# Optimization experiments

Measured on AMD Instinct MI355X. Metric: run time of the kernel, lower is better.

## Reference

```python
import jax, jax.numpy as jnp
import numpy as np

EPS = 1e-5
NEG_SLOPE = 0.2

def _conv1x1(x, w):
    # x: (B,C,N,K), w: (O,C) -> (B,O,N,K)
    return jnp.einsum('oc,bcnk->bonk', w, x)

def _bn(x, g, b, m, v):
    scale = g / jnp.sqrt(v + EPS)
    return x * scale[None, :, None, None] + (b - m * scale)[None, :, None, None]

def _lrelu(x):
    return jnp.where(x > 0, x, NEG_SLOPE * x)

def setup_inputs() -> dict:
    key = jax.random.key(0)
    specs = {
        'x': ((8, 6, 8192, 20), 'randn'),
        'trans_w': ((64, 6), 'randn'), 'trans_g': ((64,), 'rand'), 'trans_b': ((64,), 'randn'),
        'trans_m': ((64,), 'randn'), 'trans_v': ((64,), 'rand'),
        'pos_w1': ((64, 3), 'randn'), 'pos_g': ((64,), 'rand'), 'pos_b': ((64,), 'randn'),
        'pos_m': ((64,), 'randn'), 'pos_v': ((64,), 'rand'),
        'pos_w2': ((64, 64), 'randn'), 'pos_b2': ((64,), 'randn'),
        'gate_w1': ((16, 6), 'randn'), 'gate_g': ((16,), 'rand'), 'gate_b': ((16,), 'randn'),
        'gate_m': ((16,), 'randn'), 'gate_v': ((16,), 'rand'),
        'gate_w2': ((1, 16), 'randn'), 'gate_b2': ((1,), 'ones'),
        'attn_w1': ((16, 6), 'randn'), 'attn_g': ((16,), 'rand'), 'attn_b': ((16,), 'randn'),
        'attn_m': ((16,), 'randn'), 'attn_v': ((16,), 'rand'),
        'attn_w2': ((64, 16), 'randn'), 'attn_b2': ((64,), 'randn'),
    }
    out = {}
    for i, (name, (shape, fill)) in enumerate(specs.items()):
        k = jax.random.fold_in(key, i)
        if fill == 'randn':
            out[name] = jax.random.normal(k, shape, dtype=jnp.float32) * 0.1
        elif fill == 'rand':
            out[name] = jax.random.uniform(k, shape, dtype=jnp.float32)
        else:  # ones (gate bias init to 2.0 in original; scale ones)
            out[name] = jnp.ones(shape, dtype=jnp.float32) * 2.0
    return out

def reference(x, trans_w, trans_g, trans_b, trans_m, trans_v,
              pos_w1, pos_g, pos_b, pos_m, pos_v, pos_w2, pos_b2,
              gate_w1, gate_g, gate_b, gate_m, gate_v, gate_w2, gate_b2,
              attn_w1, attn_g, attn_b, attn_m, attn_v, attn_w2, attn_b2):
    in_channels = 3
    rel_pos = x[:, in_channels:in_channels + 3, :, :]  # (B,3,N,K)
    # pos_net: conv(3->C) + BN + LReLU + conv(C->C, bias)
    pos_h = _lrelu(_bn(_conv1x1(rel_pos, pos_w1), pos_g, pos_b, pos_m, pos_v))
    pos_enc = _conv1x1(pos_h, pos_w2) + pos_b2[None, :, None, None]
    # trans: conv(2*Cin->C) + BN + LReLU
    trans_feat = _lrelu(_bn(_conv1x1(x, trans_w), trans_g, trans_b, trans_m, trans_v)) + pos_enc
    # gate_net: conv(6->16)+BN+LReLU+conv(16->1,bias)+sigmoid (dropout=0 in eval)
    gate_h = _lrelu(_bn(_conv1x1(x, gate_w1), gate_g, gate_b, gate_m, gate_v))
    gate_map = jax.nn.sigmoid(_conv1x1(gate_h, gate_w2) + gate_b2[None, :, None, None])  # (B,1,N,K)
    clean_feat = trans_feat * gate_map
    # attn_net: conv(6->16)+BN+LReLU+conv(16->C,bias), then + pos_enc, softmax over K
    attn_h = _lrelu(_bn(_conv1x1(x, attn_w1), attn_g, attn_b, attn_m, attn_v))
    attn_logits = _conv1x1(attn_h, attn_w2) + attn_b2[None, :, None, None] + pos_enc
    attn_weights = jax.nn.softmax(attn_logits, axis=-1)
    out_attn = (trans_feat * attn_weights).sum(axis=-1)  # (B,C,N)
    out_max = clean_feat.max(axis=-1)                    # (B,C,N)
    return out_attn + out_max
```

## Files before the change

kernel.cpp:

```cpp
#include <hip/hip_runtime.h>
#include <math.h>

#define NEG 0.2f
#define EPSV 1e-5f

typedef _Float16 v8h __attribute__((ext_vector_type(8)));
typedef _Float16 v4h __attribute__((ext_vector_type(4)));
typedef _Float16 v2h __attribute__((ext_vector_type(2)));
typedef __fp16   f16x2 __attribute__((ext_vector_type(2)));
typedef float    v4f __attribute__((ext_vector_type(4)));

__device__ __forceinline__ float lrelu(float v) { return fmaxf(v, NEG * v); }
__device__ __forceinline__ v4f lrelu4(v4f v) {
    return __builtin_elementwise_max(v, v * NEG);
}
__device__ __forceinline__ v2h lreluh2(v2h v) {
    return __builtin_elementwise_max(v, v * (_Float16)NEG);
}

__device__ __forceinline__ v2h pk(float a, float b) {
    union { f16x2 i; v2h o; } u;
    u.i = __builtin_amdgcn_cvt_pkrtz(a, b);
    return u.o;
}

#define MFMA16(a, b, c) __builtin_amdgcn_mfma_f32_16x16x16f16((a), (b), (c), 0, 0, 0)

__global__ __launch_bounds__(256, 4)
void gsl_mfma(const float* __restrict__ x,
              const float* __restrict__ trans_w, const float* __restrict__ trans_g,
              const float* __restrict__ trans_b, const float* __restrict__ trans_m,
              const float* __restrict__ trans_v,
              const float* __restrict__ pos_w1, const float* __restrict__ pos_g,
              const float* __restrict__ pos_b, const float* __restrict__ pos_m,
              const float* __restrict__ pos_v, const float* __restrict__ pos_w2,
              const float* __restrict__ pos_b2,
              const float* __restrict__ gate_w1, const float* __restrict__ gate_g,
              const float* __restrict__ gate_b, const float* __restrict__ gate_m,
              const float* __restrict__ gate_v, const float* __restrict__ gate_w2,
              const float* __restrict__ gate_b2,
              const float* __restrict__ attn_w1, const float* __restrict__ attn_g,
              const float* __restrict__ attn_b, const float* __restrict__ attn_m,
              const float* __restrict__ attn_v, const float* __restrict__ attn_w2,
              const float* __restrict__ attn_b2,
              float* __restrict__ out)
{
    __shared__ _Float16 WH[1920];
    __shared__ _Float16 W2L[5120];
    __shared__ float    PB2[64];

    const int tid  = threadIdx.x;
    const int wv   = tid >> 6;
    const int lane = tid & 63;
    const int p    = lane & 15;
    const int q    = lane >> 4;

    const int b  = blockIdx.x >> 7;
    const int n0 = ((blockIdx.x & 127) << 6) | (wv << 4);
    const int n  = n0 | p;

    #pragma unroll
    for (int e = 0; e < 16; ++e) {
        int idx = tid * 16 + e;
        int t   = idx >> 9;
        int rem = idx & 511;
        int pp  = rem >> 5;
        int ii  = rem & 31;
        int c   = (t & 1) * 32 + ((ii & 7) >> 2) * 16 + ((ii >> 3) << 2) + (ii & 3);
        W2L[t * 640 + pp * 40 + ii] =
            (_Float16)pos_w2[((t >> 1) * 16 + pp) * 64 + c];
    }

    if (tid < 64) {
        const int c = tid;
        float sp = pos_g[c] * rsqrtf(pos_v[c] + EPSV);
        float bp = pos_b[c] - pos_m[c] * sp;
        _Float16* row = WH + (c >> 4) * 320 + (c & 15) * 20;
        for (int k = 0; k < 20; ++k) {
            float v = (k >= 3 && k < 6) ? pos_w1[c * 3 + (k - 3)] * sp
                                        : ((k == 6) ? bp : 0.f);
            row[k] = (_Float16)v;
        }
        PB2[c] = pos_b2[c];
    } else if (tid < 80) {
        const int j = tid - 64;
        float sa = attn_g[j] * rsqrtf(attn_v[j] + EPSV);
        float ba = attn_b[j] - attn_m[j] * sa;
        _Float16* row = WH + 1280 + j * 20;
        for (int k = 0; k < 20; ++k)
            row[k] = (_Float16)((k < 6) ? attn_w1[j * 6 + k] * sa
                                        : ((k == 6) ? ba : 0.f));
    } else if (tid < 96) {
        const int j = tid - 80;
        float sg = gate_g[j] * rsqrtf(gate_v[j] + EPSV);
        float bg = gate_b[j] - gate_m[j] * sg;
        _Float16* row = WH + 1600 + j * 20;
        for (int k = 0; k < 20; ++k)
            row[k] = (_Float16)((k < 6) ? gate_w1[j * 6 + k] * sg
                                        : ((k == 6) ? bg : 0.f));
    }

    v4h WTf[4], WA2f[4], WG2f;
    #pragma unroll
    for (int mt = 0; mt < 4; ++mt) {
        const int ch = mt * 16 + p;
        #pragma unroll
        for (int i = 0; i < 4; ++i)
            WA2f[mt][i] = (_Float16)attn_w2[ch * 16 + q * 4 + i];
        float st = trans_g[ch] * rsqrtf(trans_v[ch] + EPSV);
        float bt = trans_b[ch] - trans_m[ch] * st;
        #pragma unroll
        for (int i = 0; i < 4; ++i) {
            int k = q * 4 + i;
            float v = (k < 6) ? trans_w[ch * 6 + k] * st : ((k == 6) ? bt : 0.f);
            WTf[mt][i] = (_Float16)v;
        }
    }
    #pragma unroll
    for (int i = 0; i < 4; ++i)
        WG2f[i] = (_Float16)gate_w2[4 * q + i];
    const float gb2v = gate_b2[0];

    __syncthreads();

    const _Float16* const WP1p = WH + p * 20 + q * 4;
    const _Float16* const WA1p = WH + 1280 + p * 20 + q * 4;
    const _Float16* const WG1p = WH + 1600 + p * 20 + q * 4;
    const _Float16* const W2Lp = W2L + p * 40 + q * 8;
    const float* const    PB2p = PB2 + 4 * q;

    const v4f zero = {0.f, 0.f, 0.f, 0.f};
    v4f den[4], num[4], cmx[4];
    #pragma unroll
    for (int mt = 0; mt < 4; ++mt) {
        den[mt] = zero; num[mt] = zero;
        cmx[mt] = (v4f){-3.4e38f, -3.4e38f, -3.4e38f, -3.4e38f};
    }

    const float* xb = x + ((size_t)(b * 6) * 8192 + n) * 20;
    const int hi = q & 1;
    const float* const s0p = xb + (size_t)(hi ? 4 : 0) * 163840;
    const float* const s1p = xb + (size_t)(hi ? 5 : 1) * 163840;
    const float* const s2p = xb + (size_t)(hi ? 4 : 2) * 163840;
    const float* const s3p = xb + (size_t)(hi ? 5 : 3) * 163840;

    auto mk = [&](float a, float bb, float cc, float dd) -> v4h {
        v2h lo = pk(a, bb);
        v2h hh = pk(cc, dd);
        if (hi) { union { unsigned u; v2h h; } t; t.u = 0x00003C00u; hh = t.h; }
        return (v4h){lo.x, lo.y, hh.x, hh.y};
    };

    float c0 = s0p[0], c1 = s1p[0], c2 = s2p[0], c3 = s3p[0];

    #pragma unroll 1
    for (int k = 0; k < 20; ++k) {
        asm volatile("" ::: "memory");

        v4h xv = mk(c0, c1, c2, c3);
        if (k < 19) {
            c0 = s0p[k + 1]; c1 = s1p[k + 1];
            c2 = s2p[k + 1]; c3 = s3p[k + 1];
        }

        v4h phB[4];
        #pragma unroll
        for (int mt = 0; mt < 4; ++mt) {
            v4f php = MFMA16(*(const v4h*)(WP1p + mt * 320), xv, zero);
            union { v4h v; v2h h[2]; } u;
            u.h[0] = lreluh2(pk(php[0], php[1]));
            u.h[1] = lreluh2(pk(php[2], php[3]));
            phB[mt] = u.v;
        }
        v4f ahp = MFMA16(*(const v4h*)WA1p, xv, zero);
        union { v4h v; v2h h[2]; } ua;
        ua.h[0] = lreluh2(pk(ahp[0], ahp[1]));
        ua.h[1] = lreluh2(pk(ahp[2], ahp[3]));
        const v4h ahB = ua.v;

        v4f ghp = MFMA16(*(const v4h*)WG1p, xv, zero);
        union { v4h v; v2h h[2]; } ug;
        ug.h[0] = lreluh2(pk(ghp[0], ghp[1]));
        ug.h[1] = lreluh2(pk(ghp[2], ghp[3]));
        v4f gav = MFMA16(WG2f, ug.v, zero);
        const float gate = 1.f / (1.f + __expf(-(gav[0] + gb2v)));

        #pragma unroll
        for (int mt = 0; mt < 4; ++mt) {
            union { v8h v; v4h h[2]; } w2a, w2b;
            w2a.v = *(const v8h*)(W2Lp + (mt * 2 + 0) * 640);
            w2b.v = *(const v8h*)(W2Lp + (mt * 2 + 1) * 640);
            v4f pe = MFMA16(w2a.h[0], phB[0], *(const v4f*)(PB2p + mt * 16));
            pe = MFMA16(w2a.h[1], phB[1], pe);
            pe = MFMA16(w2b.h[0], phB[2], pe);
            pe = MFMA16(w2b.h[1], phB[3], pe);
            v4f tfa = MFMA16(WTf[mt], xv, zero);
            v4f tfv = lrelu4(tfa) + pe;
            pe = MFMA16(WA2f[mt], ahB, pe);
            v4f e;
            #pragma unroll
            for (int r = 0; r < 4; ++r) e[r] = __expf(pe[r]);
            den[mt] += e;
            num[mt] += tfv * e;
            cmx[mt] = __builtin_elementwise_max(cmx[mt], tfv * gate);
        }
    }

    #pragma unroll
    for (int mt = 0; mt < 4; ++mt) {
        #pragma unroll
        for (int r = 0; r < 4; ++r) {
            const int ch = mt * 16 + 4 * q + r;
            out[((size_t)(b * 64 + ch)) * 8192 + n] =
                num[mt][r] / den[mt][r] + cmx[mt][r];
        }
    }
}

extern "C" void kernel_launch(void* const* d_in, const int* in_sizes, int n_in,
                              void* d_out, int out_size, void* d_ws, size_t ws_size,
                              hipStream_t stream) {
    const float* x       = (const float*)d_in[0];
    const float* trans_w = (const float*)d_in[1];
    const float* trans_g = (const float*)d_in[2];
    const float* trans_b = (const float*)d_in[3];
    const float* trans_m = (const float*)d_in[4];
    const float* trans_v = (const float*)d_in[5];
    const float* pos_w1  = (const float*)d_in[6];
    const float* pos_g   = (const float*)d_in[7];
    const float* pos_b   = (const float*)d_in[8];
    const float* pos_m   = (const float*)d_in[9];
    const float* pos_v   = (const float*)d_in[10];
    const float* pos_w2  = (const float*)d_in[11];
    const float* pos_b2  = (const float*)d_in[12];
    const float* gate_w1 = (const float*)d_in[13];
    const float* gate_g  = (const float*)d_in[14];
    const float* gate_b  = (const float*)d_in[15];
    const float* gate_m  = (const float*)d_in[16];
    const float* gate_v  = (const float*)d_in[17];
    const float* gate_w2 = (const float*)d_in[18];
    const float* gate_b2 = (const float*)d_in[19];
    const float* attn_w1 = (const float*)d_in[20];
    const float* attn_g  = (const float*)d_in[21];
    const float* attn_b  = (const float*)d_in[22];
    const float* attn_m  = (const float*)d_in[23];
    const float* attn_v  = (const float*)d_in[24];
    const float* attn_w2 = (const float*)d_in[25];
    const float* attn_b2 = (const float*)d_in[26];
    float* out = (float*)d_out;

    gsl_mfma<<<1024, 256, 0, stream>>>(
        x, trans_w, trans_g, trans_b, trans_m, trans_v,
        pos_w1, pos_g, pos_b, pos_m, pos_v, pos_w2, pos_b2,
        gate_w1, gate_g, gate_b, gate_m, gate_v, gate_w2, gate_b2,
        attn_w1, attn_g, attn_b, attn_m, attn_v, attn_w2, attn_b2,
        out);
}
```

Baseline: 176.1 us.

## Split the K reduction across wave pairs and merge partial softmax sums via LDS

Each block now covers 32 points instead of 64. Two waves share a 16-point group and each handles half of the 20 neighbours, so the grid doubles to 2048 blocks. At the end, partial denominators, numerators and maxima are combined through an LDS buffer that reuses the weight shared memory, using extra barriers. Launch bounds are raised to 8 blocks per CU. The aim is more parallelism and shorter serial k-loops per wave. The cost is redundant weight staging per block, extra synchronisation, and register pressure from the tighter launch bound.

Result: slower. 351.5 us (+99.6%).

```diff
diff --git a/kernel.cpp b/kernel.cpp
--- a/kernel.cpp
+++ b/kernel.cpp
@@ -26,7 +26,7 @@
 
 #define MFMA16(a, b, c) __builtin_amdgcn_mfma_f32_16x16x16f16((a), (b), (c), 0, 0, 0)
 
-__global__ __launch_bounds__(256, 4)
+__global__ __launch_bounds__(256, 8)
 void gsl_mfma(const float* __restrict__ x,
               const float* __restrict__ trans_w, const float* __restrict__ trans_g,
               const float* __restrict__ trans_b, const float* __restrict__ trans_m,
@@ -45,9 +45,10 @@
               const float* __restrict__ attn_b2,
               float* __restrict__ out)
 {
-    __shared__ _Float16 WH[1920];
-    __shared__ _Float16 W2L[5120];
-    __shared__ float    PB2[64];
+    __shared__ __align__(16) char SMEM[14336];
+    _Float16* const WH  = (_Float16*)SMEM;
+    _Float16* const W2L = (_Float16*)(SMEM + 3840);
+    float*    const PB2 = (float*)(SMEM + 14080);
 
     const int tid  = threadIdx.x;
     const int wv   = tid >> 6;
@@ -55,8 +56,11 @@
     const int p    = lane & 15;
     const int q    = lane >> 4;
 
-    const int b  = blockIdx.x >> 7;
-    const int n0 = ((blockIdx.x & 127) << 6) | (wv << 4);
+    const int pw = wv & 1;
+    const int kh = wv >> 1;
+
+    const int b  = blockIdx.x >> 8;
+    const int n0 = ((blockIdx.x & 255) << 5) | (pw << 4);
     const int n  = n0 | p;
 
     #pragma unroll
@@ -151,16 +155,17 @@
         return (v4h){lo.x, lo.y, hh.x, hh.y};
     };
 
-    float c0 = s0p[0], c1 = s1p[0], c2 = s2p[0], c3 = s3p[0];
+    const int k0 = kh * 10;
+    float c0 = s0p[k0], c1 = s1p[k0], c2 = s2p[k0], c3 = s3p[k0];
 
     #pragma unroll 1
-    for (int k = 0; k < 20; ++k) {
+    for (int j = 0; j < 10; ++j) {
         asm volatile("" ::: "memory");
 
         v4h xv = mk(c0, c1, c2, c3);
-        if (k < 19) {
-            c0 = s0p[k + 1]; c1 = s1p[k + 1];
-            c2 = s2p[k + 1]; c3 = s3p[k + 1];
+        if (j < 9) {
+            const int kn = k0 + j + 1;
+            c0 = s0p[kn]; c1 = s1p[kn]; c2 = s2p[kn]; c3 = s3p[kn];
         }
 
         v4h phB[4];
@@ -206,13 +211,60 @@
         }
     }
 
-    #pragma unroll
-    for (int mt = 0; mt < 4; ++mt) {
-        #pragma unroll
-        for (int r = 0; r < 4; ++r) {
-            const int ch = mt * 16 + 4 * q + r;
-            out[((size_t)(b * 64 + ch)) * 8192 + n] =
-                num[mt][r] / den[mt][r] + cmx[mt][r];
+    __syncthreads();
+    float* const XBUF = (float*)SMEM;
+
+    if (wv == 2) {
+        float* dst = XBUF + lane * 48;
+        #pragma unroll
+        for (int mt = 0; mt < 4; ++mt) {
+            *(v4f*)(dst + mt * 4)      = den[mt];
+            *(v4f*)(dst + 16 + mt * 4) = num[mt];
+            *(v4f*)(dst + 32 + mt * 4) = cmx[mt];
+        }
+    }
+    __syncthreads();
+    if (wv == 0) {
+        const float* src = XBUF + lane * 48;
+        #pragma unroll
+        for (int mt = 0; mt < 4; ++mt) {
+            den[mt] += *(const v4f*)(src + mt * 4);
+            num[mt] += *(const v4f*)(src + 16 + mt * 4);
+            cmx[mt] = __builtin_elementwise_max(cmx[mt],
+                        *(const v4f*)(src + 32 + mt * 4));
+        }
+    }
+    __syncthreads();
+    if (wv == 3) {
+        float* dst = XBUF + lane * 48;
+        #pragma unroll
+        for (int mt = 0; mt < 4; ++mt) {
+            *(v4f*)(dst + mt * 4)      = den[mt];
+            *(v4f*)(dst + 16 + mt * 4) = num[mt];
+            *(v4f*)(dst + 32 + mt * 4) = cmx[mt];
+        }
+    }
+    __syncthreads();
+    if (wv == 1) {
+        const float* src = XBUF + lane * 48;
+        #pragma unroll
+        for (int mt = 0; mt < 4; ++mt) {
+            den[mt] += *(const v4f*)(src + mt * 4);
+            num[mt] += *(const v4f*)(src + 16 + mt * 4);
+            cmx[mt] = __builtin_elementwise_max(cmx[mt],
+                        *(const v4f*)(src + 32 + mt * 4));
+        }
+    }
+
+    if (wv < 2) {
+        #pragma unroll
+        for (int mt = 0; mt < 4; ++mt) {
+            #pragma unroll
+            for (int r = 0; r < 4; ++r) {
+                const int ch = mt * 16 + 4 * q + r;
+                out[((size_t)(b * 64 + ch)) * 8192 + n] =
+                    num[mt][r] / den[mt][r] + cmx[mt][r];
+            }
         }
     }
 }
@@ -249,7 +301,7 @@
     const float* attn_b2 = (const float*)d_in[26];
     float* out = (float*)d_out;
 
-    gsl_mfma<<<1024, 256, 0, stream>>>(
+    gsl_mfma<<<2048, 256, 0, stream>>>(
         x, trans_w, trans_g, trans_b, trans_m, trans_v,
         pos_w1, pos_g, pos_b, pos_m, pos_v, pos_w2, pos_b2,
         gate_w1, gate_g, gate_b, gate_m, gate_v, gate_w2, gate_b2,
```
